# Kernel tuning notes

Hardware: AMD Instinct MI355X
Metric: run time of the kernel (lower is better)

The kernel has to match this reference:

```python
import jax, jax.numpy as jnp
import numpy as np

NEG_INF = -1e20

def setup_inputs() -> dict:
    key = jax.random.key(0)
    kq, kk, kv, km = jax.random.split(key, 4)
    B, S, H, D = 2, 2048, 16, 64
    queries = jax.random.normal(kq, (B, S, H, D), dtype=jnp.float32)
    keys = jax.random.normal(kk, (B, S, H, D), dtype=jnp.float32)
    values = jax.random.normal(kv, (B, S, H, D), dtype=jnp.float32)
    mask = jax.random.randint(km, (B, 1, 1, S), 0, 2, dtype=jnp.int32)
    return {"queries": queries, "keys": keys, "values": values, "mask": mask}

def reference(queries, keys, values, mask):
    # scores: [B, H, Q, K]
    dk = keys.shape[-1]
    scores = jnp.einsum('bqhd,bkhd->bhqk', queries, keys) / jnp.sqrt(jnp.asarray(dk, queries.dtype))
    scores = jnp.where(mask == 0, jnp.asarray(NEG_INF, scores.dtype), scores)
    attn = jax.nn.softmax(scores, axis=-1)
    # dropout p=0.0 (eval): identity
    out = jnp.einsum('bhqv,bvhd->bqhd', attn, values)
    return out
```

## Files before the change

kernel.cpp:

```cpp
#include <hip/hip_runtime.h>
#include <hip/hip_bf16.h>

#define S_LEN 2048
#define NH 16
#define HD 64
#define KT_N 32

typedef __attribute__((ext_vector_type(8))) __bf16 bf16x8;
typedef __attribute__((ext_vector_type(16))) float f32x16;

#define QSCALE 0.1803368801111204f

static __device__ __forceinline__ ushort f2bf(float f) {
    unsigned int u = __float_as_uint(f);
    u += 0x7fffu + ((u >> 16) & 1u);
    return (ushort)(u >> 16);
}

static __device__ __forceinline__ void gload16(const void* g, void* l) {
    __builtin_amdgcn_global_load_lds(
        (const __attribute__((address_space(1))) unsigned int*)g,
        (__attribute__((address_space(3))) unsigned int*)l, 16, 0, 0);
}
static __device__ __forceinline__ void gload4(const void* g, void* l) {
    __builtin_amdgcn_global_load_lds(
        (const __attribute__((address_space(1))) unsigned int*)g,
        (__attribute__((address_space(3))) unsigned int*)l, 4, 0, 0);
}

static __device__ __forceinline__ unsigned cvtpk_bf16(float lo, float hi) {
    unsigned r;
    asm("v_cvt_pk_bf16_f32 %0, %1, %2" : "=v"(r) : "v"(lo), "v"(hi));
    return r;
}
static __device__ __forceinline__ float exp2_fast(float x) {
    float r;
    asm("v_exp_f32 %0, %1" : "=v"(r) : "v"(x));
    return r;
}

__global__ __launch_bounds__(256) void prep_k_kernel(const float* __restrict__ in,
                                                     ushort* __restrict__ out) {
    unsigned t = blockIdx.x * 256u + threadIdx.x;
    unsigned o = t & 7u;
    unsigned s = (t >> 3) & 2047u;
    unsigned bh = t >> 14;
    unsigned b = bh >> 4, h = bh & 15u;
    const float* src = in + (((size_t)(b * S_LEN) + s) * NH + h) * HD + o * 8;
    float4 x = *(const float4*)src;
    float4 y = *(const float4*)(src + 4);
    union { ushort u[8]; uint4 q; } fu;
    fu.u[0] = f2bf(x.x); fu.u[1] = f2bf(x.y); fu.u[2] = f2bf(x.z); fu.u[3] = f2bf(x.w);
    fu.u[4] = f2bf(y.x); fu.u[5] = f2bf(y.y); fu.u[6] = f2bf(y.z); fu.u[7] = f2bf(y.w);
    unsigned kt = s >> 6, kh = (s >> 5) & 1u, kl = s & 31u;
    unsigned dchunk = o >> 1, ho = o & 1u;
    size_t ci = (((size_t)(bh * 32u + kt) * 2u + kh) * 4u + dchunk) * 64u + kl + 32u * ho;
    *(uint4*)(out + ci * 8u) = fu.q;
}

__global__ __launch_bounds__(256) void prep_v_kernel(const float* __restrict__ in,
                                                     ushort* __restrict__ out) {
    __shared__ float T[64][68];
    const unsigned tid = threadIdx.x;
    const unsigned kt = blockIdx.x, bh = blockIdx.y;
    const unsigned b = bh >> 4, h = bh & 15u;
#pragma unroll
    for (int i = 0; i < 4; ++i) {
        unsigned idx = tid + i * 256u;
        unsigned sl = idx >> 4, d4 = (idx & 15u) * 4u;
        float4 v = *(const float4*)(in + (((size_t)(b * S_LEN) + kt * 64u + sl) * NH + h) * HD + d4);
        *(float4*)&T[sl][d4] = v;
    }
    __syncthreads();
#pragma unroll
    for (int it = 0; it < 2; ++it) {
        unsigned ct = tid + it * 256u;
        unsigned l = ct & 63u, sub = ct >> 6;
        unsigned nt = sub & 1u, c = (sub >> 1) & 1u, kh = sub >> 2;
        unsigned d = (l & 31u) + 32u * nt;
        unsigned kb = kh * 32u + c * 16u + (l >> 5) * 8u;
        union { ushort u[8]; uint4 q; } fu;
#pragma unroll
        for (int j = 0; j < 8; ++j) fu.u[j] = f2bf(T[kb + j][d]);
        *(uint4*)(out + ((size_t)(bh * 32u + kt) * 8u + sub) * 512u + l * 8u) = fu.q;
    }
}

__global__ __launch_bounds__(256, 2) void attn_kernel(const float* __restrict__ Qp,
                                                      const ushort* __restrict__ Kws,
                                                      const ushort* __restrict__ Vtb,
                                                      const int* __restrict__ maskp,
                                                      float* __restrict__ outp) {
    __shared__ __align__(16) ushort Kbuf[3][4096];
    __shared__ __align__(16) ushort Vbuf[3][4096];
    __shared__ __align__(16) int    mbuf[3][64];
    __shared__ float  rls[4][32];

    const unsigned tid = threadIdx.x;
    const unsigned wid = tid >> 6;
    const unsigned lane = tid & 63u;
    const unsigned l31 = lane & 31u;
    const unsigned hi = lane >> 5;

    const unsigned bh = blockIdx.y;
    const unsigned b = bh >> 4, h = bh & 15u;
    const unsigned q0 = blockIdx.x * 128u + wid * 32u;

    bf16x8 qf[4];
    {
        const float* qb = Qp + (((size_t)(b * S_LEN) + q0 + l31) * NH + h) * HD + hi * 8u;
#pragma unroll
        for (int dc = 0; dc < 4; ++dc) {
            float4 x = *(const float4*)(qb + dc * 16);
            float4 y = *(const float4*)(qb + dc * 16 + 4);
            union { ushort u[8]; bf16x8 v; } fu;
            fu.u[0] = f2bf(x.x * QSCALE); fu.u[1] = f2bf(x.y * QSCALE);
            fu.u[2] = f2bf(x.z * QSCALE); fu.u[3] = f2bf(x.w * QSCALE);
            fu.u[4] = f2bf(y.x * QSCALE); fu.u[5] = f2bf(y.y * QSCALE);
            fu.u[6] = f2bf(y.z * QSCALE); fu.u[7] = f2bf(y.w * QSCALE);
            qf[dc] = fu.v;
        }
    }

    f32x16 oacc0 = {0,0,0,0,0,0,0,0,0,0,0,0,0,0,0,0};
    f32x16 oacc1 = {0,0,0,0,0,0,0,0,0,0,0,0,0,0,0,0};
    float ls0 = 0.f, ls1 = 0.f, ls2 = 0.f, ls3 = 0.f;

    const char* kbase_g = (const char*)Kws + (size_t)bh * 262144u;
    const char* vbase_g = (const char*)Vtb + (size_t)bh * 262144u;
    const int* mb_g = maskp + (size_t)b * S_LEN;

#define STAGE(KT, PB) do {                                                        \
    unsigned seg0 = 2u * wid;                                                     \
    gload16(kbase_g + ((size_t)(KT) * 8u + seg0) * 1024u + lane * 16u,            \
            &Kbuf[PB][seg0 * 512u]);                                              \
    gload16(kbase_g + ((size_t)(KT) * 8u + seg0 + 1u) * 1024u + lane * 16u,       \
            &Kbuf[PB][(seg0 + 1u) * 512u]);                                       \
    gload16(vbase_g + ((size_t)(KT) * 8u + seg0) * 1024u + lane * 16u,            \
            &Vbuf[PB][seg0 * 512u]);                                              \
    gload16(vbase_g + ((size_t)(KT) * 8u + seg0 + 1u) * 1024u + lane * 16u,       \
            &Vbuf[PB][(seg0 + 1u) * 512u]);                                       \
    if (wid == 0) gload4(mb_g + (KT) * 64 + lane, &mbuf[PB][0]);                  \
  } while (0)

    STAGE(0, 0u);
    STAGE(1, 1u);
    asm volatile("s_waitcnt vmcnt(4)" ::: "memory");
    __builtin_amdgcn_s_barrier();

    unsigned cur = 0u, st = 2u;
    for (int i = 0; i < KT_N; ++i) {
        if (i < KT_N - 2) STAGE(i + 2, st);
        const ushort* kr = &Kbuf[cur][0];
        const ushort* vr = &Vbuf[cur][0];
        const int*    mr = &mbuf[cur][0];

#pragma unroll
        for (int kh = 0; kh < 2; ++kh) {
            bf16x8 kf[4];
#pragma unroll
            for (int dc = 0; dc < 4; ++dc)
                kf[dc] = *(const bf16x8*)&kr[(kh * 4 + dc) * 512u + lane * 8u];

            f32x16 s = {0,0,0,0,0,0,0,0,0,0,0,0,0,0,0,0};
            __builtin_amdgcn_s_setprio(1);
#pragma unroll
            for (int dc = 0; dc < 4; ++dc)
                s = __builtin_amdgcn_mfma_f32_32x32x16_bf16(kf[dc], qf[dc], s, 0, 0, 0);
            __builtin_amdgcn_s_setprio(0);

            float p[16];
#pragma unroll
            for (int r1 = 0; r1 < 4; ++r1) {
                int mv[4];
                *(int4*)mv = *(const int4*)&mr[kh * 32 + r1 * 8 + hi * 4];
#pragma unroll
                for (int r0 = 0; r0 < 4; ++r0) {
                    const int reg = r1 * 4 + r0;
                    float t = mv[r0] ? s[reg] : -1e30f;
                    p[reg] = exp2_fast(t);
                }
                ls0 += p[r1 * 4 + 0]; ls1 += p[r1 * 4 + 1];
                ls2 += p[r1 * 4 + 2]; ls3 += p[r1 * 4 + 3];
            }

#pragma unroll
            for (int c = 0; c < 2; ++c) {
                unsigned x  = cvtpk_bf16(p[8 * c + 0], p[8 * c + 1]);
                unsigned x2 = cvtpk_bf16(p[8 * c + 2], p[8 * c + 3]);
                unsigned y  = cvtpk_bf16(p[8 * c + 4], p[8 * c + 5]);
                unsigned y2 = cvtpk_bf16(p[8 * c + 6], p[8 * c + 7]);
                unsigned xs  = (unsigned)__shfl_xor((int)x, 32);
                unsigned x2s = (unsigned)__shfl_xor((int)x2, 32);
                unsigned ys  = (unsigned)__shfl_xor((int)y, 32);
                unsigned y2s = (unsigned)__shfl_xor((int)y2, 32);
                union { unsigned w[4]; bf16x8 v; } pa;
                pa.w[0] = hi ? ys  : x;
                pa.w[1] = hi ? y2s : x2;
                pa.w[2] = hi ? y   : xs;
                pa.w[3] = hi ? y2  : x2s;
                bf16x8 vf0 = *(const bf16x8*)&vr[((kh * 2 + c) * 2 + 0) * 512u + lane * 8u];
                bf16x8 vf1 = *(const bf16x8*)&vr[((kh * 2 + c) * 2 + 1) * 512u + lane * 8u];
                __builtin_amdgcn_s_setprio(1);
                oacc0 = __builtin_amdgcn_mfma_f32_32x32x16_bf16(pa.v, vf0, oacc0, 0, 0, 0);
                oacc1 = __builtin_amdgcn_mfma_f32_32x32x16_bf16(pa.v, vf1, oacc1, 0, 0, 0);
                __builtin_amdgcn_s_setprio(0);
            }
        }

        if (i < KT_N - 2) asm volatile("s_waitcnt vmcnt(4)" ::: "memory");
        else              asm volatile("s_waitcnt vmcnt(0)" ::: "memory");
        __builtin_amdgcn_s_barrier();
        cur = (cur == 2u) ? 0u : cur + 1u;
        st  = (st  == 2u) ? 0u : st  + 1u;
    }
#undef STAGE

    float lsum = (ls0 + ls1) + (ls2 + ls3);
    lsum += __shfl_xor(lsum, 32);
    if (hi == 0) rls[wid][l31] = 1.0f / lsum;
    __syncthreads();

#pragma unroll
    for (int r1 = 0; r1 < 4; ++r1) {
#pragma unroll
        for (int r0 = 0; r0 < 4; ++r0) {
            const int reg = r1 * 4 + r0;
            const unsigned q = r0 + 8u * r1 + 4u * hi;
            const float rr = rls[wid][q];
            float* ob = outp + (((size_t)(b * S_LEN) + q0 + q) * NH + h) * HD + l31;
            ob[0]  = oacc0[reg] * rr;
            ob[32] = oacc1[reg] * rr;
        }
    }
}

extern "C" void kernel_launch(void* const* d_in, const int* in_sizes, int n_in,
                              void* d_out, int out_size, void* d_ws, size_t ws_size,
                              hipStream_t stream) {
    const float* Qp = (const float*)d_in[0];
    const float* Kp = (const float*)d_in[1];
    const float* Vp = (const float*)d_in[2];
    const int* maskp = (const int*)d_in[3];
    float* outp = (float*)d_out;

    ushort* Kws = (ushort*)d_ws;
    ushort* Vws = Kws + (size_t)2 * NH * S_LEN * HD;

    hipLaunchKernelGGL(prep_k_kernel, dim3(2048), dim3(256), 0, stream, Kp, Kws);
    hipLaunchKernelGGL(prep_v_kernel, dim3(KT_N, 32), dim3(256), 0, stream, Vp, Vws);
    hipLaunchKernelGGL(attn_kernel, dim3(S_LEN / 128, 32), dim3(256), 0, stream,
                       Qp, Kws, Vws, maskp, outp);
}
```

Baseline: 76.38 us.

## Split KV range across two wave groups per block and merge partial outputs

Doubles the block to 512 threads: four query-subtile waves for each of two key halves, so each wave group walks 16 key tiles instead of 32. Each group double-buffers its own K/V/mask tiles in shared memory. Group 1 then writes its partial output and row sums into a shared buffer that reuses the tile memory through a union, and group 0 adds them before normalising. This aims to shorten the serial KV loop and raise the number of waves per CU, at the cost of an extra cross-wave reduction and a drop from triple to double buffering with a full wait each iteration.

```diff
diff --git a/kernel.cpp b/kernel.cpp
--- a/kernel.cpp
+++ b/kernel.cpp
@@ -4,7 +4,6 @@
 #define S_LEN 2048
 #define NH 16
 #define HD 64
-#define KT_N 32
 
 typedef __attribute__((ext_vector_type(8))) __bf16 bf16x8;
 typedef __attribute__((ext_vector_type(16))) float f32x16;
@@ -86,25 +85,36 @@
     }
 }
 
-__global__ __launch_bounds__(256, 2) void attn_kernel(const float* __restrict__ Qp,
+struct TileMem {
+    ushort K[2][2][4096];
+    ushort V[2][2][4096];
+    int    mb[2][2][64];
+};
+struct CombMem {
+    float ob[4][32][64];
+    float lsb[4][64];
+    float rls[4][32];
+};
+union SMemU { TileMem s; CombMem c; };
+
+__global__ __launch_bounds__(512, 4) void attn_kernel(const float* __restrict__ Qp,
                                                       const ushort* __restrict__ Kws,
-                                                      const ushort* __restrict__ Vtb,
+                                                      const ushort* __restrict__ Vws,
                                                       const int* __restrict__ maskp,
                                                       float* __restrict__ outp) {
-    __shared__ __align__(16) ushort Kbuf[3][4096];
-    __shared__ __align__(16) ushort Vbuf[3][4096];
-    __shared__ __align__(16) int    mbuf[3][64];
-    __shared__ float  rls[4][32];
+    __shared__ __align__(16) SMemU sm;
 
     const unsigned tid = threadIdx.x;
     const unsigned wid = tid >> 6;
     const unsigned lane = tid & 63u;
     const unsigned l31 = lane & 31u;
     const unsigned hi = lane >> 5;
+    const unsigned qsub = wid & 3u;
+    const unsigned kgrp = wid >> 2;
 
     const unsigned bh = blockIdx.y;
     const unsigned b = bh >> 4, h = bh & 15u;
-    const unsigned q0 = blockIdx.x * 128u + wid * 32u;
+    const unsigned q0 = blockIdx.x * 128u + qsub * 32u;
 
     bf16x8 qf[4];
     {
@@ -126,34 +136,37 @@
     f32x16 oacc1 = {0,0,0,0,0,0,0,0,0,0,0,0,0,0,0,0};
     float ls0 = 0.f, ls1 = 0.f, ls2 = 0.f, ls3 = 0.f;
 
-    const char* kbase_g = (const char*)Kws + (size_t)bh * 262144u;
-    const char* vbase_g = (const char*)Vtb + (size_t)bh * 262144u;
-    const int* mb_g = maskp + (size_t)b * S_LEN;
-
-#define STAGE(KT, PB) do {                                                        \
-    unsigned seg0 = 2u * wid;                                                     \
-    gload16(kbase_g + ((size_t)(KT) * 8u + seg0) * 1024u + lane * 16u,            \
-            &Kbuf[PB][seg0 * 512u]);                                              \
-    gload16(kbase_g + ((size_t)(KT) * 8u + seg0 + 1u) * 1024u + lane * 16u,       \
-            &Kbuf[PB][(seg0 + 1u) * 512u]);                                       \
-    gload16(vbase_g + ((size_t)(KT) * 8u + seg0) * 1024u + lane * 16u,            \
-            &Vbuf[PB][seg0 * 512u]);                                              \
-    gload16(vbase_g + ((size_t)(KT) * 8u + seg0 + 1u) * 1024u + lane * 16u,       \
-            &Vbuf[PB][(seg0 + 1u) * 512u]);                                       \
-    if (wid == 0) gload4(mb_g + (KT) * 64 + lane, &mbuf[PB][0]);                  \
+    const char* kgp = (const char*)Kws + (size_t)bh * 262144u
+                    + ((size_t)kgrp * 131072u) + (2u * qsub) * 1024u + lane * 16u;
+    const char* vgp = (const char*)Vws + (size_t)bh * 262144u
+                    + ((size_t)kgrp * 131072u) + (2u * qsub) * 1024u + lane * 16u;
+    const int* mgp = maskp + (size_t)b * S_LEN + kgrp * 1024u + lane;
+
+    ushort* klb = &sm.s.K[kgrp][0][2u * qsub * 512u];
+    ushort* vlb = &sm.s.V[kgrp][0][2u * qsub * 512u];
+    int*    mlb = &sm.s.mb[kgrp][0][0];
+    const ushort* krd = &sm.s.K[kgrp][0][0];
+    const ushort* vrd = &sm.s.V[kgrp][0][0];
+
+#define STAGE(I, PB) do {                                                      \
+    const size_t toff = (size_t)(I) * 8192u;                                   \
+    gload16(kgp + toff,          klb + (PB) * 4096u);                          \
+    gload16(kgp + toff + 1024u,  klb + (PB) * 4096u + 512u);                   \
+    gload16(vgp + toff,          vlb + (PB) * 4096u);                          \
+    gload16(vgp + toff + 1024u,  vlb + (PB) * 4096u + 512u);                   \
+    if (qsub == 0) gload4(mgp + (I) * 64, mlb + (PB) * 64u);                   \
   } while (0)
 
     STAGE(0, 0u);
-    STAGE(1, 1u);
-    asm volatile("s_waitcnt vmcnt(4)" ::: "memory");
-    __builtin_amdgcn_s_barrier();
-
-    unsigned cur = 0u, st = 2u;
-    for (int i = 0; i < KT_N; ++i) {
-        if (i < KT_N - 2) STAGE(i + 2, st);
-        const ushort* kr = &Kbuf[cur][0];
-        const ushort* vr = &Vbuf[cur][0];
-        const int*    mr = &mbuf[cur][0];
+    asm volatile("s_waitcnt vmcnt(0)" ::: "memory");
+    __syncthreads();
+
+    unsigned pb = 0;
+    for (int i = 0; i < 16; ++i) {
+        if (i < 15) STAGE(i + 1, pb ^ 1u);
+        const ushort* kr = krd + pb * 4096u;
+        const ushort* vr = vrd + pb * 4096u;
+        const int*    mr = mlb + pb * 64u;
 
 #pragma unroll
         for (int kh = 0; kh < 2; ++kh) {
@@ -207,30 +220,43 @@
                 __builtin_amdgcn_s_setprio(0);
             }
         }
-
-        if (i < KT_N - 2) asm volatile("s_waitcnt vmcnt(4)" ::: "memory");
-        else              asm volatile("s_waitcnt vmcnt(0)" ::: "memory");
-        __builtin_amdgcn_s_barrier();
-        cur = (cur == 2u) ? 0u : cur + 1u;
-        st  = (st  == 2u) ? 0u : st  + 1u;
+        asm volatile("s_waitcnt vmcnt(0)" ::: "memory");
+        __syncthreads();
+        pb ^= 1u;
     }
 #undef STAGE
 
     float lsum = (ls0 + ls1) + (ls2 + ls3);
     lsum += __shfl_xor(lsum, 32);
-    if (hi == 0) rls[wid][l31] = 1.0f / lsum;
+
+    if (kgrp == 1) {
+#pragma unroll
+        for (int r = 0; r < 16; ++r) {
+            sm.c.ob[qsub][r][lane]      = oacc0[r];
+            sm.c.ob[qsub][16 + r][lane] = oacc1[r];
+        }
+        sm.c.lsb[qsub][lane] = lsum;
+    }
     __syncthreads();
-
-#pragma unroll
-    for (int r1 = 0; r1 < 4; ++r1) {
-#pragma unroll
-        for (int r0 = 0; r0 < 4; ++r0) {
-            const int reg = r1 * 4 + r0;
-            const unsigned q = r0 + 8u * r1 + 4u * hi;
-            const float rr = rls[wid][q];
-            float* ob = outp + (((size_t)(b * S_LEN) + q0 + q) * NH + h) * HD + l31;
-            ob[0]  = oacc0[reg] * rr;
-            ob[32] = oacc1[reg] * rr;
+    if (kgrp == 0) {
+        lsum += sm.c.lsb[qsub][lane];
+#pragma unroll
+        for (int r = 0; r < 16; ++r) {
+            oacc0[r] += sm.c.ob[qsub][r][lane];
+            oacc1[r] += sm.c.ob[qsub][16 + r][lane];
+        }
+        if (hi == 0) sm.c.rls[qsub][l31] = 1.0f / lsum;
+#pragma unroll
+        for (int r1 = 0; r1 < 4; ++r1) {
+#pragma unroll
+            for (int r0 = 0; r0 < 4; ++r0) {
+                const int reg = r1 * 4 + r0;
+                const unsigned q = r0 + 8u * r1 + 4u * hi;
+                const float rr = sm.c.rls[qsub][q];
+                float* ob = outp + (((size_t)(b * S_LEN) + q0 + q) * NH + h) * HD + l31;
+                ob[0]  = oacc0[reg] * rr;
+                ob[32] = oacc1[reg] * rr;
+            }
         }
     }
 }
@@ -248,7 +274,7 @@
     ushort* Vws = Kws + (size_t)2 * NH * S_LEN * HD;
 
     hipLaunchKernelGGL(prep_k_kernel, dim3(2048), dim3(256), 0, stream, Kp, Kws);
-    hipLaunchKernelGGL(prep_v_kernel, dim3(KT_N, 32), dim3(256), 0, stream, Vp, Vws);
-    hipLaunchKernelGGL(attn_kernel, dim3(S_LEN / 128, 32), dim3(256), 0, stream,
+    hipLaunchKernelGGL(prep_v_kernel, dim3(32, 32), dim3(256), 0, stream, Vp, Vws);
+    hipLaunchKernelGGL(attn_kernel, dim3(S_LEN / 128, 32), dim3(512), 0, stream,
                        Qp, Kws, Vws, maskp, outp);
 }
```

Result: faster. 68.18 us (-10.7%).
